# Performance work log

Measured on AMD Instinct MI355X. Metric: run time of the kernel, lower is better.

The kernel has to match this reference:

```python
import jax, jax.numpy as jnp
import numpy as np

B, T, D, H = 4, 2048, 512, 8
DH = D // H
SCALE = DH ** -0.5
CAUSAL = True


def setup_inputs() -> dict:
    key = jax.random.key(0)
    k1, k2, k3, k4 = jax.random.split(key, 4)
    x = jax.random.normal(k1, (B, T, D), dtype=jnp.float32)
    # realistic padding mask: each batch element has a random valid length
    lengths = jax.random.randint(k4, (B,), T // 2, T + 1)
    m = (jnp.arange(T)[None, :] < lengths[:, None]).astype(jnp.float32)[:, :, None]  # (B,T,1)
    w_qkv = jax.random.normal(k2, (D, 3 * D), dtype=jnp.float32) * (D ** -0.5)
    w_out = jax.random.normal(k3, (D, D), dtype=jnp.float32) * (D ** -0.5)
    b_out = jnp.zeros((D,), dtype=jnp.float32)
    return {"x": x, "m": m, "w_qkv": w_qkv, "w_out": w_out, "b_out": b_out}


def reference(x, m, w_qkv, w_out, b_out):
    qkv = x @ w_qkv
    q, k, v = jnp.split(qkv, 3, axis=-1)
    q = q.reshape(B, T, H, DH)
    k = k.reshape(B, T, H, DH)
    v = v.reshape(B, T, H, DH)
    # scores: (b,i,j,h), materialized like the torch module
    e = jnp.einsum('bihd,bjhd->bijh', q, k) * SCALE
    # key-padding mask (b,i,j)
    kpm = m[:, :, None, 0] * m[:, None, :, 0]
    if CAUSAL:
        kpm = jnp.tril(kpm)
    neg = -jnp.finfo(e.dtype).max
    e = jnp.where(kpm[..., None] == 0, neg, e)
    a = jax.nn.softmax(e, axis=2)
    o = jnp.einsum('bijh,bjhd->bihd', a, v).reshape(B, T, D)
    o = o @ w_out + b_out
    return o * m
```

## Files before the change

kernel.cpp:

```cpp
#include <hip/hip_runtime.h>
#include <hip/hip_bf16.h>

#define B_   4
#define T_   2048
#define D_   512
#define H_   8
#define DH_  64
#define BT_  (B_*T_)
#define N3D_ (3*D_)

typedef __bf16  bf16x8 __attribute__((ext_vector_type(8)));
typedef float   f32x4  __attribute__((ext_vector_type(4)));
typedef short   short8 __attribute__((ext_vector_type(8)));
typedef unsigned short u16;

#if defined(__has_builtin)
#if __has_builtin(__builtin_amdgcn_exp2f)
#define EXP2_OK 1
#endif
#endif
#ifndef EXP2_OK
#define EXP2_OK 0
#endif

#if EXP2_OK
#define QSCALE_F (0.125f * 1.44269504088896340736f)
static __device__ __forceinline__ float fastexp(float x) { return __builtin_amdgcn_exp2f(x); }
#else
#define QSCALE_F (0.125f)
static __device__ __forceinline__ float fastexp(float x) { return __expf(x); }
#endif

static __device__ __forceinline__ f32x4 fzero() { f32x4 z = {0.f,0.f,0.f,0.f}; return z; }

static __device__ __forceinline__ f32x4 mfma16(short8 a, short8 b, f32x4 c) {
  return __builtin_amdgcn_mfma_f32_16x16x32_bf16(
      __builtin_bit_cast(bf16x8, a), __builtin_bit_cast(bf16x8, b), c, 0, 0, 0);
}

static __device__ __forceinline__ int swz(int byteoff) {
  return byteoff ^ (((byteoff >> 7) & 7) << 4);
}

static __device__ __forceinline__ u16 bf16bits(float f) {
  __hip_bfloat16 h = __float2bfloat16(f);
  return *reinterpret_cast<u16*>(&h);
}

static __device__ __forceinline__ void gld_lds16(const void* g, void* l) {
  __builtin_amdgcn_global_load_lds(
      (const __attribute__((address_space(1))) void*)g,
      (__attribute__((address_space(3))) void*)l, 16, 0, 0);
}

template <int N>
static __device__ __forceinline__ void vwait() {
  asm volatile("s_waitcnt vmcnt(%0)" :: "i"(N) : "memory");
}

#define XBLKS 768
__global__ __launch_bounds__(256) void prep_kernel(
    const float* __restrict__ x, const float* __restrict__ wqkv,
    const float* __restrict__ wout,
    u16* __restrict__ xb, u16* __restrict__ wqkvT, u16* __restrict__ woutT) {
  __shared__ u16 lt[64 * 72];
  const int tid = threadIdx.x;
  const int blk = blockIdx.x;

  if (blk < XBLKS) {
    const float4* x4 = reinterpret_cast<const float4*>(x);
    for (int idx = blk * 256 + tid; idx < BT_*D_/8; idx += XBLKS * 256) {
      float4 a = x4[idx*2], b = x4[idx*2+1];
      short8 o;
      o[0] = (short)bf16bits(a.x); o[1] = (short)bf16bits(a.y);
      o[2] = (short)bf16bits(a.z); o[3] = (short)bf16bits(a.w);
      o[4] = (short)bf16bits(b.x); o[5] = (short)bf16bits(b.y);
      o[6] = (short)bf16bits(b.z); o[7] = (short)bf16bits(b.w);
      *reinterpret_cast<short8*>(&xb[idx*8]) = o;
    }
    return;
  }

  int wb = blk - XBLKS;
  const float* src;
  u16* dst;
  int srcld, k0, n0;
  if (wb < 192) {
    src = wqkv; dst = wqkvT; srcld = N3D_;
    k0 = (wb & 7) * 64; n0 = (wb >> 3) * 64;
  } else {
    wb -= 192;
    src = wout; dst = woutT; srcld = D_;
    k0 = (wb & 7) * 64; n0 = (wb >> 3) * 64;
  }
  {
    int c = tid & 63, r0 = tid >> 6;
#pragma unroll
    for (int i = 0; i < 16; ++i) {
      int r = r0 * 16 + i;
      lt[r * 72 + c] = bf16bits(src[(long)(k0 + r) * srcld + n0 + c]);
    }
  }
  __syncthreads();
  {
    int kc = (tid & 7) * 8;
#pragma unroll
    for (int half = 0; half < 2; ++half) {
      int n = (tid >> 3) + half * 32;
      short8 v;
#pragma unroll
      for (int j = 0; j < 8; ++j) v[j] = (short)lt[(kc + j) * 72 + n];
      *reinterpret_cast<short8*>(&dst[(long)(n0 + n) * D_ + k0 + kc]) = v;
    }
  }
}

template <int MODE>
__global__ __launch_bounds__(256) void gemm_kernel(
    const u16* __restrict__ A, const u16* __restrict__ Wt,
    u16* __restrict__ qbuf, u16* __restrict__ kbuf, u16* __restrict__ vtbuf,
    const float* __restrict__ bias, const float* __restrict__ msk,
    float* __restrict__ out) {
  const int NBN = (MODE == 0) ? 12 : 4;
  const int lin = blockIdx.x;
  const int cpx = gridDim.x >> 3;
  const int nn = (lin & 7) * cpx + (lin >> 3);
  const int bm = nn / NBN, bn = nn % NBN;

  const int tid = threadIdx.x;
  const int w = tid >> 6, l = tid & 63;
  const int wr = w >> 1, wc = w & 1;
  const int lr = l & 15, lg = l >> 4;

  __shared__ char ls[4][16384];

  f32x4 acc[4][4];
#pragma unroll
  for (int i = 0; i < 4; ++i)
#pragma unroll
    for (int j = 0; j < 4; ++j) acc[i][j] = fzero();

  const char* Ab = reinterpret_cast<const char*>(A) + (long)bm * 128 * 1024;
  const char* Wb = reinterpret_cast<const char*>(Wt) + (long)bn * 128 * 1024;

  const int sg  = ((l >> 3) << 1) + ((l >> 2) & 1);
  const int skb = (((l & 3) ^ ((l >> 3) & 3)) << 4);

  auto stage = [&](int kt, char* dst) {
#pragma unroll
    for (int c = 0; c < 2; ++c) {
      int chunk = w * 2 + c;
      int g = chunk * 16 + sg;
      gld_lds16(Ab + (long)g * 1024 + kt * 64 + skb, dst + chunk * 1024);
      gld_lds16(Wb + (long)g * 1024 + kt * 64 + skb, dst + 8192 + chunk * 1024);
    }
  };

  auto comp = [&](const char* base) {
    const char* lsA = base;
    const char* lsB = base + 8192;
    short8 af[4], bfr[4];
#pragma unroll
    for (int mi = 0; mi < 4; ++mi) {
      int g = wr * 64 + mi * 16 + lr;
      af[mi] = *reinterpret_cast<const short8*>(
          lsA + (g >> 1) * 128 + (g & 1) * 64 + ((lg ^ ((g >> 1) & 3)) << 4));
    }
#pragma unroll
    for (int ni = 0; ni < 4; ++ni) {
      int g = wc * 64 + ni * 16 + lr;
      bfr[ni] = *reinterpret_cast<const short8*>(
          lsB + (g >> 1) * 128 + (g & 1) * 64 + ((lg ^ ((g >> 1) & 3)) << 4));
    }
    __builtin_amdgcn_s_setprio(1);
#pragma unroll
    for (int mi = 0; mi < 4; ++mi)
#pragma unroll
      for (int ni = 0; ni < 4; ++ni)
        acc[mi][ni] = mfma16(af[mi], bfr[ni], acc[mi][ni]);
    __builtin_amdgcn_s_setprio(0);
  };

  stage(0, ls[0]);
  stage(1, ls[1]);
  stage(2, ls[2]);

#define GSTEP(T, NW) { \
    vwait<NW>(); \
    __builtin_amdgcn_s_barrier(); \
    asm volatile("" ::: "memory"); \
    if ((T) + 3 < 16) stage((T) + 3, ls[((T) + 3) & 3]); \
    comp(ls[(T) & 3]); \
  }
  GSTEP(0, 8)  GSTEP(1, 8)  GSTEP(2, 8)  GSTEP(3, 8)
  GSTEP(4, 8)  GSTEP(5, 8)  GSTEP(6, 8)  GSTEP(7, 8)
  GSTEP(8, 8)  GSTEP(9, 8)  GSTEP(10, 8) GSTEP(11, 8)
  GSTEP(12, 8) GSTEP(13, 8) GSTEP(14, 4) GSTEP(15, 0)
#undef GSTEP

  if (MODE == 0) {
    char* lse = &ls[0][0];
    const int which = bn >> 2;
    if (which == 2) {
#pragma unroll
      for (int mi = 0; mi < 4; ++mi)
#pragma unroll
        for (int r = 0; r < 4; ++r) {
          int trow = wr * 64 + mi * 16 + lg * 4 + r;
#pragma unroll
          for (int ni = 0; ni < 4; ++ni) {
            int dcol = wc * 64 + ni * 16 + lr;
            int off = dcol * 256 + trow * 2;
            off ^= ((off >> 8) & 7) << 4;
            *reinterpret_cast<u16*>(lse + off) = bf16bits(acc[mi][ni][r]);
          }
        }
    } else {
      const float scale = (which == 0) ? QSCALE_F : 1.0f;
#pragma unroll
      for (int mi = 0; mi < 4; ++mi)
#pragma unroll
        for (int r = 0; r < 4; ++r) {
          int trow = wr * 64 + mi * 16 + lg * 4 + r;
#pragma unroll
          for (int ni = 0; ni < 4; ++ni) {
            int dcol = wc * 64 + ni * 16 + lr;
            int off = trow * 256 + dcol * 2;
            off ^= ((off >> 8) & 7) << 4;
            *reinterpret_cast<u16*>(lse + off) = bf16bits(acc[mi][ni][r] * scale);
          }
        }
    }
    __syncthreads();
    const int b = bm >> 4;
    const int tb0 = (bm & 15) * 128;
    if (which == 2) {
      const int bn8 = bn - 8;
#pragma unroll
      for (int it = 0; it < 8; ++it) {
        int dp = it * 16 + (tid >> 4);
        int tc = (tid & 15) * 16;
        int off = dp * 256 + (tc ^ ((dp & 7) << 4));
        short8 v = *reinterpret_cast<const short8*>(lse + off);
        int h = 2 * bn8 + (dp >> 6), d = dp & 63;
        long dst = ((long)((b * H_ + h) * DH_ + d)) * T_ + tb0 + tc / 2;
        *reinterpret_cast<short8*>(vtbuf + dst) = v;
      }
    } else {
      u16* obuf = (which == 0) ? qbuf : kbuf;
#pragma unroll
      for (int it = 0; it < 8; ++it) {
        int trow = it * 16 + (tid >> 4);
        int tc = (tid & 15) * 16;
        int off = trow * 256 + (tc ^ ((trow & 7) << 4));
        short8 v = *reinterpret_cast<const short8*>(lse + off);
        int dcol = tc / 2;
        int h = (bn & 3) * 2 + (dcol >> 6), d = dcol & 63;
        long dst = ((long)(b * H_ + h) * T_ + tb0 + trow) * DH_ + d;
        *reinterpret_cast<short8*>(obuf + dst) = v;
      }
    }
  } else {
#pragma unroll
    for (int mi = 0; mi < 4; ++mi) {
#pragma unroll
      for (int r = 0; r < 4; ++r) {
        int grow = bm * 128 + wr * 64 + mi * 16 + lg * 4 + r;
#pragma unroll
        for (int ni = 0; ni < 4; ++ni) {
          int gcol = bn * 128 + wc * 64 + ni * 16 + lr;
          float o = (acc[mi][ni][r] + bias[gcol]) * msk[grow];
          out[(long)grow * D_ + gcol] = o;
        }
      }
    }
  }
}

__global__ __launch_bounds__(512) void attn_kernel(
    const u16* __restrict__ q, const u16* __restrict__ k,
    const u16* __restrict__ vt, const float* __restrict__ msk,
    u16* __restrict__ ao) {
  const int bh = blockIdx.x;
  const int qt = 31 - blockIdx.y;
  const int b = bh >> 3, h = bh & 7;
  const int tid = threadIdx.x;
  const int w = tid >> 6;
  const int wq = w & 3;
  const int hf = w >> 2;
  const int l = tid & 63;
  const int lr = l & 15, lg = l >> 4;

  const float* mrow = msk + b * T_;

  unsigned long long bal = __ballot((l < 32) ? (mrow[l * 64] != 0.f) : false);
  const int nvalid = __popcll(bal);
  if (qt >= nvalid) return;
  const int nkv = (qt + 1 < nvalid) ? (qt + 1) : nvalid;
  const int nh = (nkv - hf + 1) >> 1;
  const int niter = (nkv + 1) >> 1;

  __shared__ char lsK[2 * 2 * 64 * 128];
  __shared__ char lsV[2 * 2 * 64 * 128];
  __shared__ char lsP[8 * 16 * 128];
  char* pbase = lsP + w * (16 * 128);
  char* myK = lsK + hf * 16384;
  char* myV = lsV + hf * 16384;

  const char* kb = reinterpret_cast<const char*>(k)  + (long)bh * T_ * 128;
  const char* vb = reinterpret_cast<const char*>(vt) + (long)bh * DH_ * T_ * 2;
  const char* qb = reinterpret_cast<const char*>(q);

  const int qrow0 = qt * 64 + wq * 16;

  short8 qf[2];
#pragma unroll
  for (int c = 0; c < 2; ++c)
    qf[c] = *reinterpret_cast<const short8*>(
        qb + (((long)bh * T_ + qrow0 + lr) * DH_ + c * 32 + lg * 8) * 2);

  const int srow = l >> 3;
  const int scol = ((l & 7) ^ srow) << 4;

  auto issue = [&](int kt_, int buf) {
#pragma unroll
    for (int c = 0; c < 2; ++c) {
      int chunk = wq * 2 + c;
      int row = chunk * 8 + srow;
      gld_lds16(kb + ((long)kt_ * 64 + row) * 128 + scol,
                myK + buf * 8192 + chunk * 1024);
      gld_lds16(vb + (long)row * (T_ * 2) + kt_ * 128 + scol,
                myV + buf * 8192 + chunk * 1024);
    }
  };

  if (0 < nh) issue(hf, 0);

  float mrun = -__builtin_inff(), lrun = 0.f;
  f32x4 oacc[4];
#pragma unroll
  for (int g = 0; g < 4; ++g) oacc[g] = fzero();

  for (int i = 0; i < niter; ++i) {
    __syncthreads();
    if (i + 1 < nh) issue(2 * (i + 1) + hf, (i + 1) & 1);
    if (i < nh) {
      const int kt = 2 * i + hf;
      const char* lk = myK + (i & 1) * 8192;
      const char* lv = myV + (i & 1) * 8192;

      f32x4 st[4];
      __builtin_amdgcn_s_setprio(1);
#pragma unroll
      for (int ni = 0; ni < 4; ++ni) {
        short8 kf0 = *reinterpret_cast<const short8*>(
            lk + swz((ni * 16 + lr) * 128 + lg * 16));
        short8 kf1 = *reinterpret_cast<const short8*>(
            lk + swz((ni * 16 + lr) * 128 + 64 + lg * 16));
        f32x4 z = fzero();
        z = mfma16(kf0, qf[0], z);
        z = mfma16(kf1, qf[1], z);
        st[ni] = z;
      }
      __builtin_amdgcn_s_setprio(0);

      const bool diag = (kt == qt);
      const bool needcm = (mrow[kt * 64 + 63] == 0.f);
      if (diag || needcm) {
#pragma unroll
        for (int ni = 0; ni < 4; ++ni)
#pragma unroll
          for (int r = 0; r < 4; ++r) {
            int jin = ni * 16 + lg * 4 + r;
            bool bad = (diag && jin > wq * 16 + lr) ||
                       (needcm && mrow[kt * 64 + jin] == 0.f);
            if (bad) st[ni][r] = -3.402823466e38f;
          }
      }

      float pmax = -3.402823466e38f;
#pragma unroll
      for (int ni = 0; ni < 4; ++ni)
#pragma unroll
        for (int r = 0; r < 4; ++r) pmax = fmaxf(pmax, st[ni][r]);
      pmax = fmaxf(pmax, __shfl_xor(pmax, 16));
      pmax = fmaxf(pmax, __shfl_xor(pmax, 32));

      if (!__all(pmax - mrun <= 8.f)) {
        float newm = fmaxf(mrun, pmax);
        float alpha = fastexp(mrun - newm);
        lrun *= alpha;
        mrun = newm;
#pragma unroll
        for (int rr = 0; rr < 4; ++rr) {
          float a = __shfl(alpha, lg * 4 + rr, 16);
#pragma unroll
          for (int g = 0; g < 4; ++g) oacc[g][rr] *= a;
        }
      }

      float p[4][4];
      float rs = 0.f;
#pragma unroll
      for (int ni = 0; ni < 4; ++ni)
#pragma unroll
        for (int r = 0; r < 4; ++r) {
          float pv = fastexp(st[ni][r] - mrun);
          p[ni][r] = pv;
          rs += pv;
        }
      rs += __shfl_xor(rs, 16);
      rs += __shfl_xor(rs, 32);
      lrun += rs;

#pragma unroll
      for (int ni = 0; ni < 4; ++ni)
#pragma unroll
        for (int rp = 0; rp < 2; ++rp) {
          unsigned lo = bf16bits(p[ni][2 * rp]);
          unsigned hi = bf16bits(p[ni][2 * rp + 1]);
          *reinterpret_cast<unsigned*>(
              pbase + swz(lr * 128 + ni * 32 + lg * 8 + rp * 4)) = lo | (hi << 16);
        }
      asm volatile("s_waitcnt lgkmcnt(0)" ::: "memory");

      __builtin_amdgcn_s_setprio(1);
#pragma unroll
      for (int c = 0; c < 2; ++c) {
        short8 pa = *reinterpret_cast<const short8*>(
            pbase + swz(lr * 128 + c * 64 + lg * 16));
#pragma unroll
        for (int g = 0; g < 4; ++g) {
          short8 vf = *reinterpret_cast<const short8*>(
              lv + swz((g * 16 + lr) * 128 + c * 64 + lg * 16));
          oacc[g] = mfma16(pa, vf, oacc[g]);
        }
      }
      __builtin_amdgcn_s_setprio(0);
    }
  }

  __syncthreads();
  float* mO  = reinterpret_cast<float*>(lsK);
  float* mML = reinterpret_cast<float*>(lsK + 4 * 4096);
  if (hf == 1) {
#pragma unroll
    for (int g = 0; g < 4; ++g)
#pragma unroll
      for (int rr = 0; rr < 4; ++rr)
        mO[wq * 1024 + (lg * 4 + rr) * 64 + g * 16 + lr] = oacc[g][rr];
    if (lg == 0) {
      mML[wq * 32 + lr * 2]     = mrun;
      mML[wq * 32 + lr * 2 + 1] = lrun;
    }
  }
  __syncthreads();
  if (hf == 0) {
    float m1 = mML[wq * 32 + lr * 2];
    float l1 = mML[wq * 32 + lr * 2 + 1];
    float M  = fmaxf(mrun, m1);
    float a0 = fastexp(mrun - M);
    float a1 = fastexp(m1 - M);
    float L  = a0 * lrun + a1 * l1;
#pragma unroll
    for (int rr = 0; rr < 4; ++rr) {
      int qrow = lg * 4 + rr;
      float a0r = __shfl(a0, qrow, 16);
      float a1r = __shfl(a1, qrow, 16);
      float Lr  = __shfl(L,  qrow, 16);
      float inv = 1.0f / Lr;
      int t = qrow0 + qrow;
#pragma unroll
      for (int g = 0; g < 4; ++g) {
        float o = a0r * oacc[g][rr] +
                  a1r * mO[wq * 1024 + qrow * 64 + g * 16 + lr];
        ao[((long)(b * T_ + t)) * D_ + h * 64 + g * 16 + lr] = bf16bits(o * inv);
      }
    }
  }
}

extern "C" void kernel_launch(void* const* d_in, const int* in_sizes, int n_in,
                              void* d_out, int out_size, void* d_ws,
                              size_t ws_size, hipStream_t stream) {
  const float* x    = (const float*)d_in[0];
  const float* msk  = (const float*)d_in[1];
  const float* wqkv = (const float*)d_in[2];
  const float* wout = (const float*)d_in[3];
  const float* bout = (const float*)d_in[4];
  float* out = (float*)d_out;

  char* ws = (char*)d_ws;
  u16* xb    = (u16*)(ws);
  u16* wqkvT = (u16*)(ws + 8388608);
  u16* woutT = (u16*)(ws + 9961472);
  u16* qbuf  = (u16*)(ws + 10485760);
  u16* kbuf  = (u16*)(ws + 18874368);
  u16* vtbuf = (u16*)(ws + 27262976);
  u16* ao    = (u16*)(ws + 35651584);

  prep_kernel<<<1024, 256, 0, stream>>>(x, wqkv, wout, xb, wqkvT, woutT);
  gemm_kernel<0><<<(N3D_ / 128) * (BT_ / 128), 256, 0, stream>>>(
      xb, wqkvT, qbuf, kbuf, vtbuf, nullptr, nullptr, nullptr);
  attn_kernel<<<dim3(B_ * H_, T_ / 64), 512, 0, stream>>>(
      qbuf, kbuf, vtbuf, msk, ao);
  gemm_kernel<1><<<(D_ / 128) * (BT_ / 128), 256, 0, stream>>>(
      ao, woutT, nullptr, nullptr, nullptr, bout, msk, out);
}
```

Measured before the change: 71.21 us.

## Skip padded row tiles in GEMMs and pass P via shuffles

Both GEMM kernels now read the padding mask at the first row of each 128-row tile and exit early when that row is padded. The output GEMM writes zeros for those tiles, which is valid because the mask is a prefix of valid positions and the output is multiplied by it. In attention, the probability tile no longer goes through LDS with a waitcnt. Register-level cross-lane shuffles rearrange it directly into the MFMA A-operand layout. The shuffles add VALU/permute work in exchange for removing LDS traffic and a sync point.

```diff
diff --git a/kernel.cpp b/kernel.cpp
--- a/kernel.cpp
+++ b/kernel.cpp
@@ -12,6 +12,7 @@
 typedef __bf16  bf16x8 __attribute__((ext_vector_type(8)));
 typedef float   f32x4  __attribute__((ext_vector_type(4)));
 typedef short   short8 __attribute__((ext_vector_type(8)));
+typedef unsigned uint4v __attribute__((ext_vector_type(4)));
 typedef unsigned short u16;
 
 #if defined(__has_builtin)
@@ -128,6 +129,17 @@
   const int bm = nn / NBN, bn = nn % NBN;
 
   const int tid = threadIdx.x;
+
+  if (msk[bm * 128] == 0.f) {
+    if (MODE == 1) {
+      long base = (long)bm * 128 * D_;
+      float4 z4 = make_float4(0.f, 0.f, 0.f, 0.f);
+      for (int i = tid; i < 128 * D_ / 4; i += 256)
+        *reinterpret_cast<float4*>(out + base + i * 4) = z4;
+    }
+    return;
+  }
+
   const int w = tid >> 6, l = tid & 63;
   const int wr = w >> 1, wc = w & 1;
   const int lr = l & 15, lg = l >> 4;
@@ -290,6 +302,7 @@
   const int hf = w >> 2;
   const int l = tid & 63;
   const int lr = l & 15, lg = l >> 4;
+  const int a_ = lg >> 1, e_ = lg & 1;
 
   const float* mrow = msk + b * T_;
 
@@ -302,8 +315,6 @@
 
   __shared__ char lsK[2 * 2 * 64 * 128];
   __shared__ char lsV[2 * 2 * 64 * 128];
-  __shared__ char lsP[8 * 16 * 128];
-  char* pbase = lsP + w * (16 * 128);
   char* myK = lsK + hf * 16384;
   char* myV = lsV + hf * 16384;
 
@@ -413,22 +424,38 @@
       rs += __shfl_xor(rs, 32);
       lrun += rs;
 
+      unsigned pk[4][2];
 #pragma unroll
       for (int ni = 0; ni < 4; ++ni)
 #pragma unroll
+        for (int rp = 0; rp < 2; ++rp)
+          pk[ni][rp] = (unsigned)bf16bits(p[ni][2 * rp]) |
+                       ((unsigned)bf16bits(p[ni][2 * rp + 1]) << 16);
+
+      unsigned paw[2][4];
+#pragma unroll
+      for (int c = 0; c < 2; ++c) {
+#pragma unroll
         for (int rp = 0; rp < 2; ++rp) {
-          unsigned lo = bf16bits(p[ni][2 * rp]);
-          unsigned hi = bf16bits(p[ni][2 * rp + 1]);
-          *reinterpret_cast<unsigned*>(
-              pbase + swz(lr * 128 + ni * 32 + lg * 8 + rp * 4)) = lo | (hi << 16);
-        }
-      asm volatile("s_waitcnt lgkmcnt(0)" ::: "memory");
+          unsigned ua = pk[2 * c][rp], ub = pk[2 * c + 1][rp];
+          unsigned st0 = e_ ? ub : ua;
+          unsigned st1 = e_ ? ua : ub;
+          int s0 = lr + 16 * ((2 * lg + a_) & 3);
+          int s1 = lr + 16 * ((2 * lg + (a_ ^ 1)) & 3);
+          unsigned g0 = (unsigned)__shfl((int)st0, s0, 64);
+          unsigned g1 = (unsigned)__shfl((int)st1, s1, 64);
+          paw[c][rp]     = a_ ? g1 : g0;
+          paw[c][2 + rp] = a_ ? g0 : g1;
+        }
+      }
 
       __builtin_amdgcn_s_setprio(1);
 #pragma unroll
       for (int c = 0; c < 2; ++c) {
-        short8 pa = *reinterpret_cast<const short8*>(
-            pbase + swz(lr * 128 + c * 64 + lg * 16));
+        uint4v pv4;
+        pv4[0] = paw[c][0]; pv4[1] = paw[c][1];
+        pv4[2] = paw[c][2]; pv4[3] = paw[c][3];
+        short8 pa = __builtin_bit_cast(short8, pv4);
 #pragma unroll
         for (int g = 0; g < 4; ++g) {
           short8 vf = *reinterpret_cast<const short8*>(
@@ -501,7 +528,7 @@
 
   prep_kernel<<<1024, 256, 0, stream>>>(x, wqkv, wout, xb, wqkvT, woutT);
   gemm_kernel<0><<<(N3D_ / 128) * (BT_ / 128), 256, 0, stream>>>(
-      xb, wqkvT, qbuf, kbuf, vtbuf, nullptr, nullptr, nullptr);
+      xb, wqkvT, qbuf, kbuf, vtbuf, nullptr, msk, nullptr);
   attn_kernel<<<dim3(B_ * H_, T_ / 64), 512, 0, stream>>>(
       qbuf, kbuf, vtbuf, msk, ao);
   gemm_kernel<1><<<(D_ / 128) * (BT_ / 128), 256, 0, stream>>>(
```

Measured after the change: 79.94 us. 1.12x slower.
